# Kernel optimization log

Measured on AMD Instinct MI355X. Metric: run time of the kernel, lower is better.

## Reference

```python
import jax, jax.numpy as jnp
import numpy as np

N = 16384      # tokens (batch 4 * seq 4096)
H = 4096       # hidden_dim
E = 64         # num_experts
P = 6          # pca_dim = log2(num_experts)
K = 8          # top_k


def setup_inputs() -> dict:
    key = jax.random.key(0)
    k1, k2, k3 = jax.random.split(key, 3)
    return {
        "x": jax.random.normal(k1, (N, H), jnp.float32),
        "pca_mean": jax.random.normal(k2, (H,), jnp.float32) * 0.02,
        "pca_components": jax.random.normal(k3, (P, H), jnp.float32) / np.sqrt(H).astype(np.float32),
        "leaf_centroids": jax.random.normal(jax.random.fold_in(key, 7), (E, P), jnp.float32),
        "top_k": K,
    }


def reference(x, pca_mean, pca_components, leaf_centroids, top_k):
    # PCA projection: (x - mean) @ components.T -> [N, P]
    proj = (x - pca_mean) @ pca_components.T
    # Euclidean cdist to centroids [E, P] via the |a|^2 - 2ab + |b|^2 expansion
    d2 = (jnp.sum(proj * proj, axis=-1, keepdims=True)
          - 2.0 * proj @ leaf_centroids.T
          + jnp.sum(leaf_centroids * leaf_centroids, axis=-1))
    dists = jnp.sqrt(jnp.maximum(d2, 0.0))            # [N, E]
    probs = jax.nn.softmax(-dists, axis=-1)           # [N, E]
    topk_probs, topk_indices = jax.lax.top_k(probs, top_k)
    topk_probs = topk_probs / jnp.sum(topk_probs, axis=-1, keepdims=True)
    return topk_indices, topk_probs, probs
```

## Files before the change

### kernel.cpp

```cpp
#include <hip/hip_runtime.h>

#define N_TOK 16384
#define H_DIM 4096
#define H4    1024
#define P_DIM 6
#define E_NUM 64
#define K_TOP 8
#define BLOCK 1024
#define WAVES 16
#define GRID  256
#define TOK_PER_BLOCK 64
#define TW 4
#define NIT (H4 / 64)

__global__
__attribute__((amdgpu_flat_work_group_size(BLOCK, BLOCK), amdgpu_waves_per_eu(4, 4)))
void kdtree_router_kernel(const float* __restrict__ x,
                          const float* __restrict__ pca_mean,
                          const float* __restrict__ pca_comp,
                          const float* __restrict__ centroids,
                          float* __restrict__ out) {
    __shared__ float4 sW4[P_DIM * H4];
    __shared__ float  sC[P_DIM * E_NUM];
    __shared__ float  sRed[WAVES * P_DIM];

    const int tid  = threadIdx.x;
    const int wave = tid >> 6;
    const int lane = tid & 63;

    const float4* Wg4   = (const float4*)pca_comp;
    const float4* mean4 = (const float4*)pca_mean;
    const float4* x4    = (const float4*)x;

    const int n0 = blockIdx.x * TOK_PER_BLOCK + wave * TW;

    float4 xc[TW];
    #pragma unroll
    for (int t = 0; t < TW; ++t) xc[t] = x4[(n0 + t) * H4 + lane];

    if (tid < E_NUM * P_DIM) {
        int e = tid / P_DIM, p = tid - e * P_DIM;
        sC[p * E_NUM + e] = centroids[tid];
    }

    const float4 m4 = mean4[tid];
    #pragma unroll
    for (int p = 0; p < P_DIM; ++p) {
        float4 w = Wg4[p * H4 + tid];
        sW4[p * H4 + tid] = w;
        float sp = w.x * m4.x + w.y * m4.y + w.z * m4.z + w.w * m4.w;
        #pragma unroll
        for (int off = 32; off > 0; off >>= 1) sp += __shfl_xor(sp, off, 64);
        if (lane == 0) sRed[wave * P_DIM + p] = sp;
    }
    __syncthreads();

    float mp[P_DIM];
    #pragma unroll
    for (int p = 0; p < P_DIM; ++p) {
        float s = 0.f;
        #pragma unroll
        for (int w = 0; w < WAVES; ++w) s += sRed[w * P_DIM + p];
        mp[p] = s;
    }

    float* out_idx = out;
    float* out_tp  = out + N_TOK * K_TOP;
    float* out_pr  = out + 2 * N_TOK * K_TOP;

    float acc[TW][P_DIM];
    #pragma unroll
    for (int t = 0; t < TW; ++t)
        #pragma unroll
        for (int p = 0; p < P_DIM; ++p) acc[t][p] = 0.f;

    for (int it = 0; it < NIT; ++it) {
        float4 xn[TW];
        if (it < NIT - 1) {
            int h4n = (it + 1) * 64 + lane;
            #pragma unroll
            for (int t = 0; t < TW; ++t) xn[t] = x4[(n0 + t) * H4 + h4n];
        }
        const int h4 = it * 64 + lane;
        float4 w[P_DIM];
        #pragma unroll
        for (int p = 0; p < P_DIM; ++p) w[p] = sW4[p * H4 + h4];

        #pragma unroll
        for (int t = 0; t < TW; ++t) {
            #pragma unroll
            for (int p = 0; p < P_DIM; ++p) {
                acc[t][p] += xc[t].x * w[p].x + xc[t].y * w[p].y
                           + xc[t].z * w[p].z + xc[t].w * w[p].w;
            }
        }
        if (it < NIT - 1) {
            #pragma unroll
            for (int t = 0; t < TW; ++t) xc[t] = xn[t];
        }
    }

    #pragma unroll
    for (int t = 0; t < TW; ++t) {
        const int n = n0 + t;
        float pr[P_DIM];
        #pragma unroll
        for (int p = 0; p < P_DIM; ++p) {
            float v = acc[t][p];
            #pragma unroll
            for (int off = 32; off > 0; off >>= 1) v += __shfl_xor(v, off, 64);
            pr[p] = v - mp[p];
        }

        float d2 = 0.f;
        #pragma unroll
        for (int p = 0; p < P_DIM; ++p) {
            float diff = pr[p] - sC[p * E_NUM + lane];
            d2 += diff * diff;
        }
        float dist = sqrtf(d2);

        float mn = dist;
        #pragma unroll
        for (int off = 32; off > 0; off >>= 1) mn = fminf(mn, __shfl_xor(mn, off, 64));
        float ev  = __expf(mn - dist);
        float sum = ev;
        #pragma unroll
        for (int off = 32; off > 0; off >>= 1) sum += __shfl_xor(sum, off, 64);
        float prob = ev / sum;
        out_pr[n * E_NUM + lane] = prob;

        float v = prob; int idx = lane;
        float tsum = 0.f, myv = 0.f; int myi = 0;
        #pragma unroll
        for (int r = 0; r < K_TOP; ++r) {
            float bv = v; int bi = idx;
            #pragma unroll
            for (int off = 32; off > 0; off >>= 1) {
                float ov = __shfl_xor(bv, off, 64);
                int   oi = __shfl_xor(bi, off, 64);
                if (ov > bv || (ov == bv && oi < bi)) { bv = ov; bi = oi; }
            }
            tsum += bv;
            if (lane == r) { myv = bv; myi = bi; }
            if (idx == bi) v = -1.f;
        }
        if (lane < K_TOP) {
            out_idx[n * K_TOP + lane] = (float)myi;
            out_tp [n * K_TOP + lane] = myv / tsum;
        }
    }
}

extern "C" void kernel_launch(void* const* d_in, const int* in_sizes, int n_in,
                              void* d_out, int out_size, void* d_ws, size_t ws_size,
                              hipStream_t stream) {
    const float* x         = (const float*)d_in[0];
    const float* pca_mean  = (const float*)d_in[1];
    const float* pca_comp  = (const float*)d_in[2];
    const float* centroids = (const float*)d_in[3];
    float* out = (float*)d_out;

    kdtree_router_kernel<<<GRID, BLOCK, 0, stream>>>(x, pca_mean, pca_comp, centroids, out);
}
```

Baseline: 415.1 us.

## Stream tokens sequentially per wave with depth-2 prefetch and interleaved epilogue

Each wave now processes its four tokens one after another instead of accumulating four tokens at once. A single float4 stream is loaded with a two-step-ahead software prefetch, and each token's softmax/top-k epilogue runs inline as soon as that token's reduction completes. Token assignment changes to interleave waves (token = block base + round*16 + wave), and the loop is kept rolled. This cuts register pressure and overlaps the epilogue with outstanding loads, but it keeps fewer independent loads in flight per wave than the four-token version did.

```diff
diff --git a/kernel.cpp b/kernel.cpp
--- a/kernel.cpp
+++ b/kernel.cpp
@@ -10,8 +10,8 @@
 #define WAVES 16
 #define GRID  256
 #define TOK_PER_BLOCK 64
-#define TW 4
-#define NIT (H4 / 64)
+#define NCH   16
+#define NSTEP 64
 
 __global__
 __attribute__((amdgpu_flat_work_group_size(BLOCK, BLOCK), amdgpu_waves_per_eu(4, 4)))
@@ -32,11 +32,10 @@
     const float4* mean4 = (const float4*)pca_mean;
     const float4* x4    = (const float4*)x;
 
-    const int n0 = blockIdx.x * TOK_PER_BLOCK + wave * TW;
+    const int base = (blockIdx.x * TOK_PER_BLOCK + wave) * H4 + lane;
 
-    float4 xc[TW];
-    #pragma unroll
-    for (int t = 0; t < TW; ++t) xc[t] = x4[(n0 + t) * H4 + lane];
+    float4 xc = x4[base];
+    float4 xn = x4[base + 64];
 
     if (tid < E_NUM * P_DIM) {
         int e = tid / P_DIM, p = tid - e * P_DIM;
@@ -68,86 +67,78 @@
     float* out_tp  = out + N_TOK * K_TOP;
     float* out_pr  = out + 2 * N_TOK * K_TOP;
 
-    float acc[TW][P_DIM];
+    float acc[P_DIM];
     #pragma unroll
-    for (int t = 0; t < TW; ++t)
-        #pragma unroll
-        for (int p = 0; p < P_DIM; ++p) acc[t][p] = 0.f;
+    for (int p = 0; p < P_DIM; ++p) acc[p] = 0.f;
 
-    for (int it = 0; it < NIT; ++it) {
-        float4 xn[TW];
-        if (it < NIT - 1) {
-            int h4n = (it + 1) * 64 + lane;
-            #pragma unroll
-            for (int t = 0; t < TW; ++t) xn[t] = x4[(n0 + t) * H4 + h4n];
-        }
-        const int h4 = it * 64 + lane;
+    #pragma unroll 1
+    for (int s = 0; s < NSTEP; ++s) {
+        const int sp2 = (s + 2 < NSTEP) ? (s + 2) : (NSTEP - 1);
+        const float4 xf = x4[base + ((sp2 >> 4) << 14) + ((sp2 & 15) << 6)];
+
+        const int c = s & 15;
         float4 w[P_DIM];
         #pragma unroll
-        for (int p = 0; p < P_DIM; ++p) w[p] = sW4[p * H4 + h4];
+        for (int p = 0; p < P_DIM; ++p) w[p] = sW4[p * H4 + c * 64 + lane];
 
         #pragma unroll
-        for (int t = 0; t < TW; ++t) {
+        for (int p = 0; p < P_DIM; ++p) {
+            acc[p] += xc.x * w[p].x + xc.y * w[p].y
+                    + xc.z * w[p].z + xc.w * w[p].w;
+        }
+        xc = xn;
+        xn = xf;
+
+        if (c == NCH - 1) {
+            const int n = blockIdx.x * TOK_PER_BLOCK + (s >> 4) * WAVES + wave;
+
+            float pr[P_DIM];
             #pragma unroll
             for (int p = 0; p < P_DIM; ++p) {
-                acc[t][p] += xc[t].x * w[p].x + xc[t].y * w[p].y
-                           + xc[t].z * w[p].z + xc[t].w * w[p].w;
+                float v = acc[p];
+                #pragma unroll
+                for (int off = 32; off > 0; off >>= 1) v += __shfl_xor(v, off, 64);
+                pr[p] = v - mp[p];
+                acc[p] = 0.f;
             }
-        }
-        if (it < NIT - 1) {
+
+            float d2 = 0.f;
             #pragma unroll
-            for (int t = 0; t < TW; ++t) xc[t] = xn[t];
-        }
-    }
+            for (int p = 0; p < P_DIM; ++p) {
+                float diff = pr[p] - sC[p * E_NUM + lane];
+                d2 += diff * diff;
+            }
+            float dist = sqrtf(d2);
 
-    #pragma unroll
-    for (int t = 0; t < TW; ++t) {
-        const int n = n0 + t;
-        float pr[P_DIM];
-        #pragma unroll
-        for (int p = 0; p < P_DIM; ++p) {
-            float v = acc[t][p];
+            float mn = dist;
             #pragma unroll
-            for (int off = 32; off > 0; off >>= 1) v += __shfl_xor(v, off, 64);
-            pr[p] = v - mp[p];
-        }
+            for (int off = 32; off > 0; off >>= 1) mn = fminf(mn, __shfl_xor(mn, off, 64));
+            float ev  = __expf(mn - dist);
+            float sum = ev;
+            #pragma unroll
+            for (int off = 32; off > 0; off >>= 1) sum += __shfl_xor(sum, off, 64);
+            float prob = ev / sum;
+            out_pr[n * E_NUM + lane] = prob;
 
-        float d2 = 0.f;
-        #pragma unroll
-        for (int p = 0; p < P_DIM; ++p) {
-            float diff = pr[p] - sC[p * E_NUM + lane];
-            d2 += diff * diff;
-        }
-        float dist = sqrtf(d2);
-
-        float mn = dist;
-        #pragma unroll
-        for (int off = 32; off > 0; off >>= 1) mn = fminf(mn, __shfl_xor(mn, off, 64));
-        float ev  = __expf(mn - dist);
-        float sum = ev;
-        #pragma unroll
-        for (int off = 32; off > 0; off >>= 1) sum += __shfl_xor(sum, off, 64);
-        float prob = ev / sum;
-        out_pr[n * E_NUM + lane] = prob;
-
-        float v = prob; int idx = lane;
-        float tsum = 0.f, myv = 0.f; int myi = 0;
-        #pragma unroll
-        for (int r = 0; r < K_TOP; ++r) {
-            float bv = v; int bi = idx;
+            float v = prob; int idx = lane;
+            float tsum = 0.f, myv = 0.f; int myi = 0;
             #pragma unroll
-            for (int off = 32; off > 0; off >>= 1) {
-                float ov = __shfl_xor(bv, off, 64);
-                int   oi = __shfl_xor(bi, off, 64);
-                if (ov > bv || (ov == bv && oi < bi)) { bv = ov; bi = oi; }
+            for (int r = 0; r < K_TOP; ++r) {
+                float bv = v; int bi = idx;
+                #pragma unroll
+                for (int off = 32; off > 0; off >>= 1) {
+                    float ov = __shfl_xor(bv, off, 64);
+                    int   oi = __shfl_xor(bi, off, 64);
+                    if (ov > bv || (ov == bv && oi < bi)) { bv = ov; bi = oi; }
+                }
+                tsum += bv;
+                if (lane == r) { myv = bv; myi = bi; }
+                if (idx == bi) v = -1.f;
             }
-            tsum += bv;
-            if (lane == r) { myv = bv; myi = bi; }
-            if (idx == bi) v = -1.f;
-        }
-        if (lane < K_TOP) {
-            out_idx[n * K_TOP + lane] = (float)myi;
-            out_tp [n * K_TOP + lane] = myv / tsum;
+            if (lane < K_TOP) {
+                out_idx[n * K_TOP + lane] = (float)myi;
+                out_tp [n * K_TOP + lane] = myv / tsum;
+            }
         }
     }
 }
```

Result: faster. 376.2 us (-9.4%).
